# Performance work log

Measured on AMD Instinct MI355X. Metric: run time of the kernel, lower is better.

Reference implementation:

```python
import jax, jax.numpy as jnp
import numpy as np

H = 16          # n_heads
EPS = 1e-3      # keras LayerNormalization default epsilon


def _layernorm(x, gamma, beta):
    m = jnp.mean(x, axis=-1, keepdims=True)
    v = jnp.var(x, axis=-1, keepdims=True)
    return (x - m) * jax.lax.rsqrt(v + EPS) * gamma + beta


def _mha(q, k, v, wq, bq, wk, bk, wv, bv, wo, bo, causal):
    B, Sq, D = q.shape
    Sk = k.shape[1]
    d = D // H
    qh = (q @ wq + bq).reshape(B, Sq, H, d)
    kh = (k @ wk + bk).reshape(B, Sk, H, d)
    vh = (v @ wv + bv).reshape(B, Sk, H, d)
    scores = jnp.einsum('bqhd,bkhd->bhqk', qh, kh) / jnp.sqrt(jnp.asarray(d, qh.dtype))
    if causal:
        mask = jnp.tril(jnp.ones((Sq, Sk), dtype=bool))
        scores = jnp.where(mask, scores, jnp.asarray(-1e9, scores.dtype))
    attn = jax.nn.softmax(scores, axis=-1)
    out = jnp.einsum('bhqk,bkhd->bqhd', attn, vh).reshape(B, Sq, D)
    return out @ wo + bo


def setup_inputs() -> dict:
    key = jax.random.key(0)
    B, S, D, DFF = 4, 1024, 1024, 4096
    ks = jax.random.split(key, 16)
    sc = 0.02
    inp = {
        'inputs': jax.random.normal(ks[0], (B, S, D), jnp.float32),
        'enc_outputs': jax.random.normal(ks[1], (B, S, D), jnp.float32),
    }
    # self-attention (mha1)
    inp['wq1'] = jax.random.normal(ks[2], (D, D), jnp.float32) * sc
    inp['wk1'] = jax.random.normal(ks[3], (D, D), jnp.float32) * sc
    inp['wv1'] = jax.random.normal(ks[4], (D, D), jnp.float32) * sc
    inp['wo1'] = jax.random.normal(ks[5], (D, D), jnp.float32) * sc
    inp['bq1'] = jnp.zeros((D,), jnp.float32)
    inp['bk1'] = jnp.zeros((D,), jnp.float32)
    inp['bv1'] = jnp.zeros((D,), jnp.float32)
    inp['bo1'] = jnp.zeros((D,), jnp.float32)
    # cross-attention (mha2)
    inp['wq2'] = jax.random.normal(ks[6], (D, D), jnp.float32) * sc
    inp['wk2'] = jax.random.normal(ks[7], (D, D), jnp.float32) * sc
    inp['wv2'] = jax.random.normal(ks[8], (D, D), jnp.float32) * sc
    inp['wo2'] = jax.random.normal(ks[9], (D, D), jnp.float32) * sc
    inp['bq2'] = jnp.zeros((D,), jnp.float32)
    inp['bk2'] = jnp.zeros((D,), jnp.float32)
    inp['bv2'] = jnp.zeros((D,), jnp.float32)
    inp['bo2'] = jnp.zeros((D,), jnp.float32)
    # FFN
    inp['w_ff1'] = jax.random.normal(ks[10], (D, DFF), jnp.float32) * sc
    inp['b_ff1'] = jnp.zeros((DFF,), jnp.float32)
    inp['w_ff2'] = jax.random.normal(ks[11], (DFF, D), jnp.float32) * sc
    inp['b_ff2'] = jnp.zeros((D,), jnp.float32)
    # LayerNorms
    for i in (1, 2, 3):
        inp[f'g{i}'] = jnp.ones((D,), jnp.float32)
        inp[f'be{i}'] = jnp.zeros((D,), jnp.float32)
    return inp


def reference(inputs, enc_outputs,
              wq1, bq1, wk1, bk1, wv1, bv1, wo1, bo1,
              wq2, bq2, wk2, bk2, wv2, bv2, wo2, bo2,
              w_ff1, b_ff1, w_ff2, b_ff2,
              g1, be1, g2, be2, g3, be3):
    # self-attention block (causal) + residual + LN; dropout is identity (eval)
    a1 = _mha(inputs, inputs, inputs, wq1, bq1, wk1, bk1, wv1, bv1, wo1, bo1, causal=True)
    o1 = _layernorm(inputs + a1, g1, be1)
    # cross-attention block + residual + LN
    a2 = _mha(o1, enc_outputs, enc_outputs, wq2, bq2, wk2, bk2, wv2, bv2, wo2, bo2, causal=False)
    o2 = _layernorm(o1 + a2, g2, be2)
    # FFN block + residual + LN
    f = jax.nn.relu(o2 @ w_ff1 + b_ff1) @ w_ff2 + b_ff2
    return _layernorm(o2 + f, g3, be3)
```

## Files before the change

### kernel.cpp

```cpp
#include <hip/hip_runtime.h>
#include <stdint.h>
#include <stddef.h>

typedef __attribute__((ext_vector_type(4))) float  floatx4;
typedef __attribute__((ext_vector_type(8))) short  short8;
typedef __attribute__((ext_vector_type(4))) short  short4v;

__device__ __forceinline__ float bf2f(short s) {
  union { uint32_t u; float f; } v;
  v.u = ((uint32_t)(uint16_t)s) << 16;
  return v.f;
}
__device__ __forceinline__ short f2bf(float f) {
  union { float f; uint32_t u; } v; v.f = f;
  uint32_t r = v.u + 0x7fffu + ((v.u >> 16) & 1u);
  return (short)(r >> 16);
}

__device__ __forceinline__ void async_cp16(const void* g, void* l) {
  __builtin_amdgcn_global_load_lds(
      (__attribute__((address_space(1))) void*)g,
      (__attribute__((address_space(3))) void*)l, 16, 0, 0);
}

__device__ __forceinline__ int swzb(int row, int bcol) {
  return ((row << 7) + bcol) ^ ((row & 7) << 4);
}

struct TransTable {
  const float* src[10];
  short*       dst[10];
  int K[10], N[10], base[10];
};
__global__ __launch_bounds__(256)
void transpose_all(TransTable tt)
{
  __shared__ short tile[32][33];
  int e = 0;
  #pragma unroll
  for (int i = 1; i < 10; i++) if ((int)blockIdx.x >= tt.base[i]) e = i;
  const int t = blockIdx.x - tt.base[e];
  const int N = tt.N[e], K = tt.K[e];
  const int ncols = N >> 5;
  const int n0 = (t % ncols) << 5, k0 = (t / ncols) << 5;
  const float* src = tt.src[e];
  short* dst = tt.dst[e];
  const int tx = threadIdx.x & 31, ty = threadIdx.x >> 5;
  #pragma unroll
  for (int i = 0; i < 32; i += 8)
    tile[ty + i][tx] = f2bf(src[(size_t)(k0 + ty + i) * N + n0 + tx]);
  __syncthreads();
  #pragma unroll
  for (int i = 0; i < 32; i += 8)
    dst[(size_t)(n0 + ty + i) * K + k0 + tx] = tile[tx][ty + i];
}

__global__ __launch_bounds__(256)
void convert_xe(const float* __restrict__ x, const float* __restrict__ enc,
                short* __restrict__ xc, short* __restrict__ encc)
{
  int b = blockIdx.x;
  const float* s; short* d;
  if (b < 4096) { s = x; d = xc; } else { s = enc; d = encc; b -= 4096; }
  const int i = (b * 256 + threadIdx.x) * 4;
  const floatx4 v = *(const floatx4*)(s + i);
  short4v o;
  #pragma unroll
  for (int j = 0; j < 4; j++) o[j] = f2bf(v[j]);
  *(short4v*)(d + i) = o;
}

struct ParamMap { const float* s[19]; int off[19]; };
__global__ __launch_bounds__(256)
void convert_params(ParamMap pm, short* __restrict__ dst)
{
  const int b = blockIdx.x;
  for (int t = threadIdx.x; t < 1024; t += 256)
    dst[b * 1024 + t] = f2bf(pm.s[b][pm.off[b] + t]);
}

template<int RELU, int RESID, int BM, int BN>
__global__ __launch_bounds__(256)
void gemm_bt(const short* __restrict__ A, const short* __restrict__ BT,
             const short* __restrict__ bias, const short* __restrict__ resid,
             short* __restrict__ C, int M, int N, int K)
{
  constexpr int MT = BM / 32;
  constexpr int NT = BN / 32;
  __shared__ short8 As0[BM * 4];
  __shared__ short8 As1[BM * 4];
  __shared__ short8 Bs0[BN * 4];
  __shared__ short8 Bs1[BN * 4];
  const int tid  = threadIdx.x;
  const int w    = tid >> 6;
  const int lane = tid & 63;
  const int m16  = lane & 15;
  const int g    = lane >> 4;
  const int nbn  = N / BN;
  const int bid  = ((int)blockIdx.x & 7) * ((int)gridDim.x >> 3) + ((int)blockIdx.x >> 3);
  const int bm   = bid / nbn;
  const int bn   = bid % nbn;
  const int wm   = (w >> 1) * (BM / 2);
  const int wn   = (w & 1) * (BN / 2);

  const int r0 = lane >> 2;
  const int c0 = lane & 3;
  const int csw = c0 ^ ((r0 >> 1) & 3);
  const short* pA = A  + (size_t)(bm * BM + w * (BM / 4) + r0) * K + csw * 8;
  const short* pB = BT + (size_t)(bn * BN + w * (BN / 4) + r0) * K + csw * 8;

  floatx4 acc[MT][NT];
  #pragma unroll
  for (int i = 0; i < MT; i++)
    #pragma unroll
    for (int j = 0; j < NT; j++)
      acc[i][j] = floatx4{0.f, 0.f, 0.f, 0.f};

  auto stage = [&](short8* AS, short8* BS, int k0) {
    async_cp16(pA + k0, AS + w * BM);
    if constexpr (BM == 128) async_cp16(pA + k0 + 16 * (size_t)K, AS + w * BM + 64);
    async_cp16(pB + k0, BS + w * BN);
    if constexpr (BN == 128) async_cp16(pB + k0 + 16 * (size_t)K, BS + w * BN + 64);
  };
  const int sR = (m16 >> 1) & 3;
  const int gs = g ^ sR;
  auto compute = [&](const short8* AS, const short8* BS) {
    short8 af[MT], bfr[NT];
    #pragma unroll
    for (int mt = 0; mt < MT; mt++)
      af[mt] = AS[(wm + mt * 16 + m16) * 4 + gs];
    #pragma unroll
    for (int nt = 0; nt < NT; nt++)
      bfr[nt] = BS[(wn + nt * 16 + m16) * 4 + gs];
    #pragma unroll
    for (int mt = 0; mt < MT; mt++)
      #pragma unroll
      for (int nt = 0; nt < NT; nt++)
        acc[mt][nt] = __builtin_amdgcn_mfma_f32_16x16x32_bf16(af[mt], bfr[nt], acc[mt][nt], 0, 0, 0);
  };

  stage(As0, Bs0, 0);
  __syncthreads();

  for (int k0 = 0; k0 < K; k0 += 64) {
    stage(As1, Bs1, k0 + 32);
    compute(As0, Bs0);
    __syncthreads();
    if (k0 + 64 < K)
      stage(As0, Bs0, k0 + 64);
    compute(As1, Bs1);
    __syncthreads();
  }

  #pragma unroll
  for (int mt = 0; mt < MT; mt++) {
    const int rbase = bm * BM + wm + mt * 16 + g * 4;
    #pragma unroll
    for (int nt = 0; nt < NT; nt++) {
      const int col = bn * BN + wn + nt * 16 + m16;
      const float bia = bf2f(bias[col]);
      #pragma unroll
      for (int r = 0; r < 4; r++) {
        const size_t idx = (size_t)(rbase + r) * N + col;
        float v = acc[mt][nt][r] + bia;
        if (RESID) v += bf2f(resid[idx]);
        if (RELU)  v = fmaxf(v, 0.f);
        C[idx] = f2bf(v);
      }
    }
  }
}

template<int CAUSAL>
__global__ __launch_bounds__(256, 4)
void attention(const short* __restrict__ Qp, int ldq,
               const short* __restrict__ Kp, int ldk,
               const short* __restrict__ Vp, int ldv,
               short* __restrict__ Op, int ldo)
{
  const int S   = 1024;
  const int bid = blockIdx.x;
  const int qt  = bid & 15;
  const int h   = (bid >> 4) & 15;
  const int b   = bid >> 8;
  const int tid = threadIdx.x;
  const int w   = tid >> 6;
  const int lane = tid & 63;
  const int m16 = lane & 15;
  const int g   = lane >> 4;

  __shared__ __align__(16) short Ks[2][64 * 64];
  __shared__ __align__(16) short VT[2][64 * 64];
  __shared__ __align__(16) short Ps[4][16 * 64];

  const int rowQ = b * S + qt * 64;
  const int wrow = w * 16;

  const short* qsrc = Qp + (size_t)(rowQ + wrow + m16) * ldq + h * 64 + 8 * g;
  const short8 qf0 = *(const short8*)qsrc;
  const short8 qf1 = *(const short8*)(qsrc + 32);

  float mrow = -1e38f;
  float lrow = 0.f;
  floatx4 oacc[4];
  #pragma unroll
  for (int dt = 0; dt < 4; dt++) oacc[dt] = floatx4{0.f, 0.f, 0.f, 0.f};

  const int kr  = tid >> 2, kc = (tid & 3) << 4;
  const int vkp = (tid & 31) * 2, vcg = (tid >> 5) << 3;

  const short* kbase = Kp + (size_t)(b * S + kr)  * ldk + h * 64 + kc;
  const short* vbase = Vp + (size_t)(b * S + vkp) * ldv + h * 64 + vcg;

  const int nkt = CAUSAL ? (qt + 1) : (S / 64);
  const int qi  = qt * 64 + wrow + m16;

  short8 kst0 = *(const short8*)kbase;
  short8 kst1 = *(const short8*)(kbase + 8);
  short8 vst0 = *(const short8*)vbase;
  short8 vst1 = *(const short8*)(vbase + ldv);
  {
    char* kd = (char*)&Ks[0][0];
    *(short8*)(kd + swzb(kr, kc * 2))      = kst0;
    *(short8*)(kd + swzb(kr, kc * 2 + 16)) = kst1;
    char* vd = (char*)&VT[0][0];
    #pragma unroll
    for (int j = 0; j < 8; j++) {
      const uint32_t pk = (uint32_t)(uint16_t)vst0[j] | ((uint32_t)(uint16_t)vst1[j] << 16);
      *(uint32_t*)(vd + swzb(vcg + j, vkp * 2)) = pk;
    }
  }
  __syncthreads();

  for (int kt = 0; kt < nkt; kt++) {
    const int cur  = kt & 1;
    const int more = (kt + 1 < nkt);

    if (more) {
      const size_t roff = (size_t)(kt + 1) * 64;
      kst0 = *(const short8*)(kbase + roff * ldk);
      kst1 = *(const short8*)(kbase + roff * ldk + 8);
      vst0 = *(const short8*)(vbase + roff * ldv);
      vst1 = *(const short8*)(vbase + roff * ldv + ldv);
    }

    const int kb = kt * 64;

    const char* ksrc = (const char*)&Ks[cur][0];
    floatx4 sc[4];
    #pragma unroll
    for (int cg4 = 0; cg4 < 4; cg4++) {
      const short8 kfa = *(const short8*)(ksrc + swzb(cg4 * 16 + m16, 16 * g));
      const short8 kfb = *(const short8*)(ksrc + swzb(cg4 * 16 + m16, 64 + 16 * g));
      sc[cg4] = __builtin_amdgcn_mfma_f32_16x16x32_bf16(kfa, qf0, floatx4{0.f,0.f,0.f,0.f}, 0, 0, 0);
      sc[cg4] = __builtin_amdgcn_mfma_f32_16x16x32_bf16(kfb, qf1, sc[cg4], 0, 0, 0);
    }

    float v4[4][4];
    #pragma unroll
    for (int cg = 0; cg < 4; cg++)
      #pragma unroll
      for (int r = 0; r < 4; r++) {
        float x = sc[cg][r] * 0.125f;
        if (CAUSAL && kt == qt) {
          const int key = kb + cg * 16 + g * 4 + r;
          if (key > qi) x = -1e9f;
        }
        v4[cg][r] = x;
      }

    float mx = v4[0][0];
    #pragma unroll
    for (int cg = 0; cg < 4; cg++)
      #pragma unroll
      for (int r = 0; r < 4; r++) mx = fmaxf(mx, v4[cg][r]);
    mx = fmaxf(mx, __shfl_xor(mx, 16));
    mx = fmaxf(mx, __shfl_xor(mx, 32));
    const float mn = fmaxf(mrow, mx);
    const float alpha = __expf(mrow - mn);
    mrow = mn;

    float rs = 0.f;
    #pragma unroll
    for (int cg = 0; cg < 4; cg++)
      #pragma unroll
      for (int r = 0; r < 4; r++) { v4[cg][r] = __expf(v4[cg][r] - mn); rs += v4[cg][r]; }
    rs += __shfl_xor(rs, 16);
    rs += __shfl_xor(rs, 32);
    lrow = lrow * alpha + rs;

    #pragma unroll
    for (int r = 0; r < 4; r++) {
      const float aR = __shfl(alpha, (g << 2) | r);
      #pragma unroll
      for (int dt = 0; dt < 4; dt++) oacc[dt][r] *= aR;
    }

    char* pbase = (char*)&Ps[w][0];
    #pragma unroll
    for (int cg = 0; cg < 4; cg++) {
      const uint32_t p0 = (uint32_t)(uint16_t)f2bf(v4[cg][0]) |
                          ((uint32_t)(uint16_t)f2bf(v4[cg][1]) << 16);
      const uint32_t p1 = (uint32_t)(uint16_t)f2bf(v4[cg][2]) |
                          ((uint32_t)(uint16_t)f2bf(v4[cg][3]) << 16);
      *(uint32_t*)(pbase + swzb(m16, (8 * cg + 2 * g) * 4))     = p0;
      *(uint32_t*)(pbase + swzb(m16, (8 * cg + 2 * g + 1) * 4)) = p1;
    }

    asm volatile("s_waitcnt lgkmcnt(0)" ::: "memory");
    __builtin_amdgcn_sched_barrier(0);

    const short8 pf0 = *(const short8*)(pbase + swzb(m16, 16 * g));
    const short8 pf1 = *(const short8*)(pbase + swzb(m16, 64 + 16 * g));
    const char* vsrc = (const char*)&VT[cur][0];
    #pragma unroll
    for (int dt = 0; dt < 4; dt++) {
      const short8 vfa = *(const short8*)(vsrc + swzb(dt * 16 + m16, 16 * g));
      const short8 vfb = *(const short8*)(vsrc + swzb(dt * 16 + m16, 64 + 16 * g));
      oacc[dt] = __builtin_amdgcn_mfma_f32_16x16x32_bf16(pf0, vfa, oacc[dt], 0, 0, 0);
      oacc[dt] = __builtin_amdgcn_mfma_f32_16x16x32_bf16(pf1, vfb, oacc[dt], 0, 0, 0);
    }

    if (more) {
      char* kd = (char*)&Ks[cur ^ 1][0];
      *(short8*)(kd + swzb(kr, kc * 2))      = kst0;
      *(short8*)(kd + swzb(kr, kc * 2 + 16)) = kst1;
      char* vd = (char*)&VT[cur ^ 1][0];
      #pragma unroll
      for (int j = 0; j < 8; j++) {
        const uint32_t pk = (uint32_t)(uint16_t)vst0[j] | ((uint32_t)(uint16_t)vst1[j] << 16);
        *(uint32_t*)(vd + swzb(vcg + j, vkp * 2)) = pk;
      }
      __syncthreads();
    }
  }

  float lR[4];
  #pragma unroll
  for (int r = 0; r < 4; r++) lR[r] = __shfl(lrow, (g << 2) | r);
  #pragma unroll
  for (int dt = 0; dt < 4; dt++)
    #pragma unroll
    for (int r = 0; r < 4; r++) {
      const size_t orow = (size_t)(rowQ + wrow + g * 4 + r);
      Op[orow * ldo + h * 64 + dt * 16 + m16] = f2bf(oacc[dt][r] / lR[r]);
    }
}

template<int FINAL>
__global__ __launch_bounds__(256)
void layernorm_bf16(const short* __restrict__ x, const short* __restrict__ gamma,
                    const short* __restrict__ beta, void* __restrict__ out)
{
  const int D = 1024;
  const int row = blockIdx.x, tid = threadIdx.x;
  const short* xr = x + (size_t)row * D;
  short4v xv = *(const short4v*)(xr + tid * 4);
  float v[4], s = 0.f, ss = 0.f;
  #pragma unroll
  for (int j = 0; j < 4; j++) { v[j] = bf2f(xv[j]); s += v[j]; ss += v[j] * v[j]; }
  #pragma unroll
  for (int off = 32; off; off >>= 1) { s += __shfl_xor(s, off); ss += __shfl_xor(ss, off); }
  __shared__ float red[8];
  const int w = tid >> 6, lane = tid & 63;
  if (lane == 0) { red[w] = s; red[4 + w] = ss; }
  __syncthreads();
  s  = red[0] + red[1] + red[2] + red[3];
  ss = red[4] + red[5] + red[6] + red[7];
  const float mean = s * (1.f / D);
  const float var  = ss * (1.f / D) - mean * mean;
  const float inv  = rsqrtf(var + 1e-3f);
  float o[4];
  #pragma unroll
  for (int j = 0; j < 4; j++)
    o[j] = (v[j] - mean) * inv * bf2f(gamma[tid * 4 + j]) + bf2f(beta[tid * 4 + j]);
  if (FINAL) {
    floatx4 ov;
    #pragma unroll
    for (int j = 0; j < 4; j++) ov[j] = o[j];
    *(floatx4*)((float*)out + (size_t)row * D + tid * 4) = ov;
  } else {
    short4v ov;
    #pragma unroll
    for (int j = 0; j < 4; j++) ov[j] = f2bf(o[j]);
    *(short4v*)((short*)out + (size_t)row * D + tid * 4) = ov;
  }
}

extern "C" void kernel_launch(void* const* d_in, const int* in_sizes, int n_in,
                              void* d_out, int out_size, void* d_ws, size_t ws_size,
                              hipStream_t stream) {
  (void)in_sizes; (void)n_in; (void)out_size; (void)ws_size;
  const int M = 4096;
  const size_t MM = 1024 * 1024;

  short* ws = (short*)d_ws;
  short* wt_qkv1 = ws;
  short* wt_o1   = wt_qkv1 + 3 * MM;
  short* wt_q2   = wt_o1 + MM;
  short* wt_kv2  = wt_q2 + MM;
  short* wt_o2   = wt_kv2 + 2 * MM;
  short* wt_ff1  = wt_o2 + MM;
  short* wt_ff2  = wt_ff1 + 4 * MM;
  short* P       = ws + 16 * MM;
  short* encc    = ws + 16 * MM + 32768;
  short* act0    = encc + 4 * MM;
  short* attn    = act0 + 16 * MM;
  short* t1      = attn + 4 * MM;
  short* t2      = t1 + 4 * MM;
  short* xc      = t2;

  short* bqkv1 = P,        *bo1  = P + 3072, *bkv2 = P + 4096, *bq2 = P + 6144;
  short* bo2   = P + 7168, *bff1 = P + 8192, *bff2 = P + 12288;
  short* g1 = P + 13312, *be1 = P + 14336, *g2 = P + 15360, *be2 = P + 16384;
  short* g3 = P + 17408, *be3 = P + 18432;

  ParamMap pm;
  const int srcidx[19] = {6, 7, 8, 9, 15, 16, 14, 17, 19, 19, 19, 19, 21, 22, 23, 24, 25, 26, 27};
  const int offs[19]   = {0, 0, 0, 0, 0,  0,  0,  0,  0, 1024, 2048, 3072, 0, 0, 0, 0, 0, 0, 0};
  for (int i = 0; i < 19; i++) { pm.s[i] = (const float*)d_in[srcidx[i]]; pm.off[i] = offs[i]; }
  convert_params<<<19, 256, 0, stream>>>(pm, P);

  convert_xe<<<8192, 256, 0, stream>>>((const float*)d_in[0], (const float*)d_in[1], xc, encc);

  TransTable tt;
  const int widx[10] = {2, 3, 4, 5, 10, 11, 12, 13, 18, 20};
  short* wdst[10] = {wt_qkv1, wt_qkv1 + MM, wt_qkv1 + 2 * MM, wt_o1, wt_q2,
                     wt_kv2, wt_kv2 + MM, wt_o2, wt_ff1, wt_ff2};
  const int wK[10] = {1024, 1024, 1024, 1024, 1024, 1024, 1024, 1024, 1024, 4096};
  const int wN[10] = {1024, 1024, 1024, 1024, 1024, 1024, 1024, 1024, 4096, 1024};
  int base = 0;
  for (int i = 0; i < 10; i++) {
    tt.src[i] = (const float*)d_in[widx[i]];
    tt.dst[i] = wdst[i];
    tt.K[i] = wK[i]; tt.N[i] = wN[i]; tt.base[i] = base;
    base += (wN[i] / 32) * (wK[i] / 32);
  }
  transpose_all<<<base, 256, 0, stream>>>(tt);

  short* qkv1 = act0;
  gemm_bt<0, 0, 128, 128><<<dim3((M / 128) * (3072 / 128)), 256, 0, stream>>>(
      xc, wt_qkv1, bqkv1, nullptr, qkv1, M, 3072, 1024);
  attention<1><<<dim3(1024), 256, 0, stream>>>(
      qkv1, 3072, qkv1 + 1024, 3072, qkv1 + 2048, 3072, attn, 1024);
  gemm_bt<0, 1, 64, 64><<<dim3((M / 64) * (1024 / 64)), 256, 0, stream>>>(
      attn, wt_o1, bo1, xc, t1, M, 1024, 1024);
  layernorm_bf16<0><<<dim3(4096), 256, 0, stream>>>(t1, g1, be1, t1);

  short* kv2 = act0;
  short* q2  = act0 + 8 * MM;
  gemm_bt<0, 0, 64, 128><<<dim3((M / 64) * (2048 / 128)), 256, 0, stream>>>(
      encc, wt_kv2, bkv2, nullptr, kv2, M, 2048, 1024);
  gemm_bt<0, 0, 64, 64><<<dim3((M / 64) * (1024 / 64)), 256, 0, stream>>>(
      t1, wt_q2, bq2, nullptr, q2, M, 1024, 1024);
  attention<0><<<dim3(1024), 256, 0, stream>>>(
      q2, 1024, kv2, 2048, kv2 + 1024, 2048, attn, 1024);
  gemm_bt<0, 1, 64, 64><<<dim3((M / 64) * (1024 / 64)), 256, 0, stream>>>(
      attn, wt_o2, bo2, t1, t2, M, 1024, 1024);
  layernorm_bf16<0><<<dim3(4096), 256, 0, stream>>>(t2, g2, be2, t2);

  short* hidden = act0;
  gemm_bt<1, 0, 128, 128><<<dim3((M / 128) * (4096 / 128)), 256, 0, stream>>>(
      t2, wt_ff1, bff1, nullptr, hidden, M, 4096, 1024);
  gemm_bt<0, 1, 64, 64><<<dim3((M / 64) * (1024 / 64)), 256, 0, stream>>>(
      hidden, wt_ff2, bff2, t2, attn, M, 1024, 4096);
  layernorm_bf16<1><<<dim3(4096), 256, 0, stream>>>(attn, g3, be3, d_out);
}
```

Baseline: 513.8 us.

## Add 4-stage async-copy pipelined 64x64 GEMM with vmcnt waits and block swizzle

Adds a dedicated 64x64-tile GEMM that keeps four LDS buffers in flight. It waits with fine-grained s_waitcnt vmcnt plus a barrier instead of a full __syncthreads after each double-buffered stage. It also remaps block indices across 8 groups to change L2 locality. The aim is to hide global load latency in the four 64x64 GEMMs (output projections, q2, FFN2), at the cost of more LDS per block and hand-written inline-asm synchronisation.

```diff
diff --git a/kernel.cpp b/kernel.cpp
--- a/kernel.cpp
+++ b/kernel.cpp
@@ -22,6 +22,11 @@
       (__attribute__((address_space(1))) void*)g,
       (__attribute__((address_space(3))) void*)l, 16, 0, 0);
 }
+
+#define WAITB(N) do {                                        \
+  asm volatile("s_waitcnt vmcnt(" #N ")" ::: "memory");      \
+  __builtin_amdgcn_s_barrier();                              \
+  __builtin_amdgcn_sched_barrier(0); } while (0)
 
 __device__ __forceinline__ int swzb(int row, int bcol) {
   return ((row << 7) + bcol) ^ ((row & 7) << 4);
@@ -122,8 +127,7 @@
     async_cp16(pB + k0, BS + w * BN);
     if constexpr (BN == 128) async_cp16(pB + k0 + 16 * (size_t)K, BS + w * BN + 64);
   };
-  const int sR = (m16 >> 1) & 3;
-  const int gs = g ^ sR;
+  const int gs = g ^ ((m16 >> 1) & 3);
   auto compute = [&](const short8* AS, const short8* BS) {
     short8 af[MT], bfr[NT];
     #pragma unroll
@@ -158,6 +162,93 @@
     #pragma unroll
     for (int nt = 0; nt < NT; nt++) {
       const int col = bn * BN + wn + nt * 16 + m16;
+      const float bia = bf2f(bias[col]);
+      #pragma unroll
+      for (int r = 0; r < 4; r++) {
+        const size_t idx = (size_t)(rbase + r) * N + col;
+        float v = acc[mt][nt][r] + bia;
+        if (RESID) v += bf2f(resid[idx]);
+        if (RELU)  v = fmaxf(v, 0.f);
+        C[idx] = f2bf(v);
+      }
+    }
+  }
+}
+
+template<int RELU, int RESID>
+__global__ __launch_bounds__(256)
+void gemm_bt64(const short* __restrict__ A, const short* __restrict__ BT,
+               const short* __restrict__ bias, const short* __restrict__ resid,
+               short* __restrict__ C, int M, int N, int K)
+{
+  __shared__ short8 As0[256], As1[256], As2[256], As3[256];
+  __shared__ short8 Bs0[256], Bs1[256], Bs2[256], Bs3[256];
+  const int tid  = threadIdx.x;
+  const int w    = tid >> 6;
+  const int lane = tid & 63;
+  const int m16  = lane & 15;
+  const int g    = lane >> 4;
+  const int nbn  = N >> 6;
+  const int bid  = ((int)blockIdx.x & 7) * ((int)gridDim.x >> 3) + ((int)blockIdx.x >> 3);
+  const int bm   = bid / nbn;
+  const int bn   = bid % nbn;
+  const int wm   = (w >> 1) << 5;
+  const int wn   = (w & 1) << 5;
+
+  const int r0 = lane >> 2;
+  const int c0 = lane & 3;
+  const int csw = c0 ^ ((r0 >> 1) & 3);
+  const short* pA = A  + (size_t)(bm * 64 + w * 16 + r0) * K + csw * 8;
+  const short* pB = BT + (size_t)(bn * 64 + w * 16 + r0) * K + csw * 8;
+
+  floatx4 acc[2][2];
+  #pragma unroll
+  for (int i = 0; i < 2; i++)
+    #pragma unroll
+    for (int j = 0; j < 2; j++)
+      acc[i][j] = floatx4{0.f, 0.f, 0.f, 0.f};
+
+  auto stage = [&](short8* AS, short8* BS, int k0) {
+    async_cp16(pA + k0, AS + w * 64);
+    async_cp16(pB + k0, BS + w * 64);
+  };
+  const int gs = g ^ ((m16 >> 1) & 3);
+  auto compute = [&](const short8* AS, const short8* BS) {
+    short8 af[2], bfr[2];
+    #pragma unroll
+    for (int mt = 0; mt < 2; mt++)
+      af[mt] = AS[(wm + mt * 16 + m16) * 4 + gs];
+    #pragma unroll
+    for (int nt = 0; nt < 2; nt++)
+      bfr[nt] = BS[(wn + nt * 16 + m16) * 4 + gs];
+    #pragma unroll
+    for (int mt = 0; mt < 2; mt++)
+      #pragma unroll
+      for (int nt = 0; nt < 2; nt++)
+        acc[mt][nt] = __builtin_amdgcn_mfma_f32_16x16x32_bf16(af[mt], bfr[nt], acc[mt][nt], 0, 0, 0);
+  };
+
+  stage(As0, Bs0, 0);
+  stage(As1, Bs1, 32);
+
+  int k0 = 0;
+  for (; k0 + 256 <= K; k0 += 128) {
+    stage(As2, Bs2, k0 + 64);  WAITB(4); compute(As0, Bs0);
+    stage(As3, Bs3, k0 + 96);  WAITB(4); compute(As1, Bs1);
+    stage(As0, Bs0, k0 + 128); WAITB(4); compute(As2, Bs2);
+    stage(As1, Bs1, k0 + 160); WAITB(4); compute(As3, Bs3);
+  }
+  stage(As2, Bs2, k0 + 64);  WAITB(4); compute(As0, Bs0);
+  stage(As3, Bs3, k0 + 96);  WAITB(4); compute(As1, Bs1);
+  WAITB(2); compute(As2, Bs2);
+  WAITB(0); compute(As3, Bs3);
+
+  #pragma unroll
+  for (int mt = 0; mt < 2; mt++) {
+    const int rbase = bm * 64 + wm + mt * 16 + g * 4;
+    #pragma unroll
+    for (int nt = 0; nt < 2; nt++) {
+      const int col = bn * 64 + wn + nt * 16 + m16;
       const float bia = bf2f(bias[col]);
       #pragma unroll
       for (int r = 0; r < 4; r++) {
@@ -443,7 +534,7 @@
       xc, wt_qkv1, bqkv1, nullptr, qkv1, M, 3072, 1024);
   attention<1><<<dim3(1024), 256, 0, stream>>>(
       qkv1, 3072, qkv1 + 1024, 3072, qkv1 + 2048, 3072, attn, 1024);
-  gemm_bt<0, 1, 64, 64><<<dim3((M / 64) * (1024 / 64)), 256, 0, stream>>>(
+  gemm_bt64<0, 1><<<dim3((M / 64) * (1024 / 64)), 256, 0, stream>>>(
       attn, wt_o1, bo1, xc, t1, M, 1024, 1024);
   layernorm_bf16<0><<<dim3(4096), 256, 0, stream>>>(t1, g1, be1, t1);
 
@@ -451,18 +542,18 @@
   short* q2  = act0 + 8 * MM;
   gemm_bt<0, 0, 64, 128><<<dim3((M / 64) * (2048 / 128)), 256, 0, stream>>>(
       encc, wt_kv2, bkv2, nullptr, kv2, M, 2048, 1024);
-  gemm_bt<0, 0, 64, 64><<<dim3((M / 64) * (1024 / 64)), 256, 0, stream>>>(
+  gemm_bt64<0, 0><<<dim3((M / 64) * (1024 / 64)), 256, 0, stream>>>(
       t1, wt_q2, bq2, nullptr, q2, M, 1024, 1024);
   attention<0><<<dim3(1024), 256, 0, stream>>>(
       q2, 1024, kv2, 2048, kv2 + 1024, 2048, attn, 1024);
-  gemm_bt<0, 1, 64, 64><<<dim3((M / 64) * (1024 / 64)), 256, 0, stream>>>(
+  gemm_bt64<0, 1><<<dim3((M / 64) * (1024 / 64)), 256, 0, stream>>>(
       attn, wt_o2, bo2, t1, t2, M, 1024, 1024);
   layernorm_bf16<0><<<dim3(4096), 256, 0, stream>>>(t2, g2, be2, t2);
 
   short* hidden = act0;
   gemm_bt<1, 0, 128, 128><<<dim3((M / 128) * (4096 / 128)), 256, 0, stream>>>(
       t2, wt_ff1, bff1, nullptr, hidden, M, 4096, 1024);
-  gemm_bt<0, 1, 64, 64><<<dim3((M / 64) * (1024 / 64)), 256, 0, stream>>>(
+  gemm_bt64<0, 1><<<dim3((M / 64) * (1024 / 64)), 256, 0, stream>>>(
       hidden, wt_ff2, bff2, t2, attn, M, 1024, 4096);
   layernorm_bf16<1><<<dim3(4096), 256, 0, stream>>>(attn, g3, be3, d_out);
 }
```

Measured after the change: 522.0 us. About the same (+1.6%).
